# Optimization experiments

Hardware: AMD Instinct MI355X
Metric: run time of the kernel (lower is better)

## Reference

```python
import jax, jax.numpy as jnp
from jax import lax
import numpy as np

N_NODES = 50000
N_EDGES = 800000
IN_CH = 128
HEADS = 4
OUT_CH = 32
TOP_K = 8


def setup_inputs() -> dict:
    key = jax.random.key(0)
    k1, k2, k3, k4 = jax.random.split(key, 4)
    x = jax.random.normal(k1, (N_NODES, IN_CH), jnp.float32)
    edge_index = jax.random.randint(k2, (2, N_EDGES), 0, N_NODES, dtype=jnp.int32)
    scale = float(np.sqrt(2.0 / (IN_CH + HEADS * OUT_CH)))  # xavier-ish
    W = jax.random.normal(k3, (IN_CH, HEADS * OUT_CH), jnp.float32) * scale
    att = jax.random.normal(k4, (HEADS, 2 * OUT_CH), jnp.float32) * 0.1
    return {"x": x, "W": W, "att": att, "edge_index": edge_index}


def _topk_mask_1h(e_h, row, k):
    # e_h: [E'] scores for one head; keep top-k scores within each row-segment.
    E = e_h.shape[0]
    order = jnp.lexsort((-e_h, row))          # grouped by row, descending score
    srow = row[order]
    seg_start = jnp.searchsorted(srow, srow, side="left")
    pos_in_seg = jnp.arange(E, dtype=seg_start.dtype) - seg_start
    keep_sorted = pos_in_seg < k
    return jnp.zeros((E,), jnp.bool_).at[order].set(keep_sorted)


def reference(x, W, att, edge_index):
    N = x.shape[0]
    H, C = HEADS, OUT_CH
    h = (x @ W).reshape(N, H, C)              # [N,H,C]
    # add self loops
    loops = jnp.arange(N, dtype=edge_index.dtype)
    ei = jnp.concatenate([edge_index, jnp.stack([loops, loops])], axis=1)
    row, col = ei[0], ei[1]                   # [E']
    x_i = h[row]                              # [E',H,C] gather (dst)
    x_j = h[col]                              # [E',H,C] gather (src)
    a_i, a_j = att[:, :C], att[:, C:]
    e = jnp.einsum("ehc,hc->eh", x_i, a_i) + jnp.einsum("ehc,hc->eh", x_j, a_j)
    e = jax.nn.leaky_relu(e, negative_slope=0.2)  # [E',H]
    mask = jax.vmap(lambda eh: _topk_mask_1h(eh, row, TOP_K),
                    in_axes=1, out_axes=1)(e)     # [E',H] bool
    e = jnp.where(mask, e, -jnp.inf)
    # segment softmax over rows (every node has a self loop -> non-empty segment)
    seg_max = jax.ops.segment_max(e, row, num_segments=N)
    ez = jnp.exp(e - lax.stop_gradient(seg_max)[row])  # masked edges -> 0
    denom = jax.ops.segment_sum(ez, row, num_segments=N)
    alpha = ez / denom[row]                   # [E',H]
    # dropout is identity in eval mode
    out = jax.ops.segment_sum(alpha[:, :, None] * x_j, row, num_segments=N)
    out = out.reshape(N, H * C)               # concat=True
    return jax.nn.elu(out)
```

## Files before the change

### kernel.cpp

```cpp
#include <hip/hip_runtime.h>
#include <math.h>

typedef unsigned int u32;
typedef unsigned long long u64;

#define NN 50000
#define NE 800000
#define TOPK 8
#define NB 196
#define BCAP 4608
#define CURSTRIDE 16
#define GTILES 782
#define PBLOCKS 391

__global__ __launch_bounds__(256) void gemm_k(const float* __restrict__ x,
                                              const float* __restrict__ W,
                                              const float* __restrict__ att,
                                              float* __restrict__ hbuf,
                                              float* __restrict__ s_i,
                                              float* __restrict__ s_j,
                                              int* __restrict__ cursor) {
    __shared__ float xst[64][68];
    __shared__ float ws[64][128];
    const int t = threadIdx.x;
    const int cx = t & 15;
    const int ry = t >> 4;
    const int rbase = blockIdx.x * 64;

    if (blockIdx.x == 0 && t < NB) cursor[t * CURSTRIDE] = 0;

    float acc[4][8];
    #pragma unroll
    for (int i = 0; i < 4; ++i)
        #pragma unroll
        for (int j = 0; j < 8; ++j) acc[i][j] = 0.f;

    for (int kk = 0; kk < 128; kk += 64) {
        if (kk) __syncthreads();
        #pragma unroll
        for (int rr = ry; rr < 64; rr += 16) {
            int gr = rbase + rr;
            float4 v = make_float4(0.f, 0.f, 0.f, 0.f);
            if (gr < NN)
                v = *reinterpret_cast<const float4*>(x + (size_t)gr * 128 + kk + cx * 4);
            xst[cx * 4 + 0][rr] = v.x;
            xst[cx * 4 + 1][rr] = v.y;
            xst[cx * 4 + 2][rr] = v.z;
            xst[cx * 4 + 3][rr] = v.w;
        }
        #pragma unroll
        for (int wk = t >> 5; wk < 64; wk += 8) {
            float4 v = *reinterpret_cast<const float4*>(W + (size_t)(kk + wk) * 128 + (t & 31) * 4);
            *reinterpret_cast<float4*>(&ws[wk][(t & 31) * 4]) = v;
        }
        __syncthreads();

        for (int k = 0; k < 64; ++k) {
            float4 xa = *reinterpret_cast<const float4*>(&xst[k][ry * 4]);
            float4 wa = *reinterpret_cast<const float4*>(&ws[k][cx * 8]);
            float4 wb = *reinterpret_cast<const float4*>(&ws[k][cx * 8 + 4]);
            float xv[4] = {xa.x, xa.y, xa.z, xa.w};
            float wv[8] = {wa.x, wa.y, wa.z, wa.w, wb.x, wb.y, wb.z, wb.w};
            #pragma unroll
            for (int i = 0; i < 4; ++i)
                #pragma unroll
                for (int j = 0; j < 8; ++j) acc[i][j] += xv[i] * wv[j];
        }
    }

    const int head = cx >> 2;
    float aiv[8], ajv[8];
    #pragma unroll
    for (int j = 0; j < 8; ++j) {
        aiv[j] = att[head * 64 + (cx & 3) * 8 + j];
        ajv[j] = att[head * 64 + 32 + (cx & 3) * 8 + j];
    }
    #pragma unroll
    for (int i = 0; i < 4; ++i) {
        int gr = rbase + ry * 4 + i;
        float pi = 0.f, pj = 0.f;
        #pragma unroll
        for (int j = 0; j < 8; ++j) {
            pi += acc[i][j] * aiv[j];
            pj += acc[i][j] * ajv[j];
        }
        pi += __shfl_xor(pi, 1); pi += __shfl_xor(pi, 2);
        pj += __shfl_xor(pj, 1); pj += __shfl_xor(pj, 2);
        if (gr < NN) {
            float* dst = hbuf + (size_t)gr * 128 + cx * 8;
            *reinterpret_cast<float4*>(dst)     = make_float4(acc[i][0], acc[i][1], acc[i][2], acc[i][3]);
            *reinterpret_cast<float4*>(dst + 4) = make_float4(acc[i][4], acc[i][5], acc[i][6], acc[i][7]);
            if ((cx & 3) == 0) {
                s_i[(size_t)gr * 4 + head] = pi;
                s_j[(size_t)gr * 4 + head] = pj;
            }
        }
    }
}

__global__ __launch_bounds__(256) void part_k(const int* __restrict__ ei,
                                              int* __restrict__ cursor,
                                              u32* __restrict__ breg) {
    __shared__ u32 cnt[NB];
    __shared__ u32 base[NB];
    const int t = threadIdx.x;
    if (t < NB) cnt[t] = 0;
    __syncthreads();

    const int e0 = blockIdx.x * 2048 + t * 8;
    const bool ev = e0 < NE;
    int rows[8], cols[8], bk[8];
    u32 lrk[8];
    if (ev) {
        int4 ra = *reinterpret_cast<const int4*>(ei + e0);
        int4 rb = *reinterpret_cast<const int4*>(ei + e0 + 4);
        int4 ca = *reinterpret_cast<const int4*>(ei + NE + e0);
        int4 cb = *reinterpret_cast<const int4*>(ei + NE + e0 + 4);
        rows[0] = ra.x; rows[1] = ra.y; rows[2] = ra.z; rows[3] = ra.w;
        rows[4] = rb.x; rows[5] = rb.y; rows[6] = rb.z; rows[7] = rb.w;
        cols[0] = ca.x; cols[1] = ca.y; cols[2] = ca.z; cols[3] = ca.w;
        cols[4] = cb.x; cols[5] = cb.y; cols[6] = cb.z; cols[7] = cb.w;
        #pragma unroll
        for (int i = 0; i < 8; ++i) {
            bk[i] = rows[i] >> 8;
            lrk[i] = atomicAdd(&cnt[bk[i]], 1u);
        }
    }
    __syncthreads();
    if (t < NB) base[t] = (cnt[t] > 0) ? (u32)atomicAdd(cursor + t * CURSTRIDE, (int)cnt[t]) : 0u;
    __syncthreads();
    if (ev) {
        #pragma unroll
        for (int i = 0; i < 8; ++i) {
            u32 pos = base[bk[i]] + lrk[i];
            if (pos < BCAP)
                breg[(size_t)bk[i] * BCAP + pos] = ((u32)(rows[i] & 255) << 16) | (u32)cols[i];
        }
    }
}

__global__ __launch_bounds__(256) void rowsel_k(const int* __restrict__ cursor,
                                                const u32* __restrict__ breg,
                                                const float* __restrict__ s_i,
                                                const float* __restrict__ s_j,
                                                const float* __restrict__ hbuf,
                                                float* __restrict__ out) {
    __shared__ u32 lcsr[64][65];
    __shared__ u32 ldeg[64];
    __shared__ float lal[256 * 8];
    __shared__ int   lcl[256 * 8];
    const int t = threadIdx.x;
    const int B = blockIdx.x >> 2;
    const int s = blockIdx.x & 3;
    const int rbase = B * 256 + s * 64;

    if (t < 64) ldeg[t] = 0;
    __syncthreads();

    int n = cursor[B * CURSTRIDE];
    if (n > BCAP) n = BCAP;
    const u32* reg = breg + (size_t)B * BCAP;
    for (int i = t; i < n; i += 256) {
        u32 e = reg[i];
        if ((int)(e >> 22) == s) {
            int lr = (int)((e >> 16) & 63);
            u32 rk = atomicAdd(&ldeg[lr], 1u);
            if (rk < 64) lcsr[lr][rk] = e & 0xFFFFu;
        }
    }
    __syncthreads();

    const int lrow = t >> 2;
    const int head = t & 3;
    const int row = rbase + lrow;

    u64 kl[TOPK];
    int cl[TOPK];
    #pragma unroll
    for (int i = 0; i < TOPK; ++i) { kl[i] = 0ull; cl[i] = 0; }

    int dgr = 0;
    if (row < NN) {
        dgr = (int)ldeg[lrow];
        if (dgr > 64) dgr = 64;
        float v = s_j[(size_t)row * 4 + head];
        u32 b = __float_as_uint(v);
        u32 fk = (b & 0x80000000u) ? ~b : (b | 0x80000000u);
        kl[0] = ((u64)fk << 32) | (u32)(~(u32)(NE + row));
        cl[0] = row;
    }

    for (int j = 0; j < dgr; ++j) {
        int col = (int)lcsr[lrow][j];
        float v = s_j[(size_t)col * 4 + head];
        u32 b = __float_as_uint(v);
        u32 fk = (b & 0x80000000u) ? ~b : (b | 0x80000000u);
        u64 key = ((u64)fk << 32) | (u32)(~(u32)j);
        int cc = col;
        if (key > kl[TOPK - 1]) {
            #pragma unroll
            for (int i = 0; i < TOPK; ++i) {
                bool gt = key > kl[i];
                u64 tk = gt ? kl[i] : key;  kl[i] = gt ? key : kl[i];  key = tk;
                int tc = gt ? cl[i] : cc;   cl[i] = gt ? cc : cl[i];   cc = tc;
            }
        }
    }

    {
        float si = (row < NN) ? s_i[(size_t)row * 4 + head] : 0.f;
        u32 fk = (u32)(kl[0] >> 32);
        u32 b = (fk & 0x80000000u) ? (fk ^ 0x80000000u) : ~fk;
        float vmax = __uint_as_float(b);
        float em = si + vmax;
        float m = (em >= 0.f) ? em : 0.2f * em;
        float al[TOPK];
        float denom = 0.f;
        #pragma unroll
        for (int i = 0; i < TOPK; ++i) {
            u32 fki = (u32)(kl[i] >> 32);
            u32 bi = (fki & 0x80000000u) ? (fki ^ 0x80000000u) : ~fki;
            float v = __uint_as_float(bi);
            float e = si + v;
            e = (e >= 0.f) ? e : 0.2f * e;
            float z = (kl[i] != 0ull) ? __expf(e - m) : 0.f;
            al[i] = z;
            denom += z;
        }
        float inv = 1.f / denom;
        #pragma unroll
        for (int i = 0; i < TOPK; ++i) {
            lal[t * 8 + i] = al[i] * inv;
            lcl[t * 8 + i] = cl[i];
        }
    }
    __syncthreads();

    const int lane = t & 63;
    const int wid = t >> 6;
    const int q = lane >> 3;
    const int dq = lane & 7;
    for (int g = wid; g < 32; g += 4) {
        const int p = g * 8 + q;
        const int r = rbase + (p >> 2);
        const int hh = p & 3;
        if (r < NN) {
            const int base = p * 8;
            float av[8]; int cv[8];
            #pragma unroll
            for (int k = 0; k < 8; ++k) { av[k] = lal[base + k]; cv[k] = lcl[base + k]; }
            float4 a4 = make_float4(0.f, 0.f, 0.f, 0.f);
            #pragma unroll
            for (int k = 0; k < 8; ++k) {
                const float4 hv = *reinterpret_cast<const float4*>(
                    &hbuf[(size_t)cv[k] * 128 + hh * 32 + dq * 4]);
                a4.x += av[k] * hv.x;
                a4.y += av[k] * hv.y;
                a4.z += av[k] * hv.z;
                a4.w += av[k] * hv.w;
            }
            a4.x = (a4.x > 0.f) ? a4.x : expm1f(a4.x);
            a4.y = (a4.y > 0.f) ? a4.y : expm1f(a4.y);
            a4.z = (a4.z > 0.f) ? a4.z : expm1f(a4.z);
            a4.w = (a4.w > 0.f) ? a4.w : expm1f(a4.w);
            *reinterpret_cast<float4*>(&out[(size_t)r * 128 + hh * 32 + dq * 4]) = a4;
        }
    }
}

extern "C" void kernel_launch(void* const* d_in, const int* in_sizes, int n_in,
                              void* d_out, int out_size, void* d_ws, size_t ws_size,
                              hipStream_t stream) {
    const float* x   = (const float*)d_in[0];
    const float* W   = (const float*)d_in[1];
    const float* att = (const float*)d_in[2];
    const int*   ei  = (const int*)d_in[3];
    float* out = (float*)d_out;

    u32* breg    = (u32*)d_ws;
    float* hbuf  = (float*)(breg + (size_t)NB * BCAP);
    float* s_i   = hbuf + 6400000;
    float* s_j   = s_i + 200000;
    int* cursor  = (int*)(s_j + 200000);

    gemm_k<<<GTILES, 256, 0, stream>>>(x, W, att, hbuf, s_i, s_j, cursor);
    part_k<<<PBLOCKS, 256, 0, stream>>>(ei, cursor, breg);
    rowsel_k<<<NB * 4, 256, 0, stream>>>(cursor, breg, s_i, s_j, hbuf, out);
}
```

Before: 173.6 us.

## Fuse edge partitioning into GEMM kernel and shrink shared index arrays to u16

Edge bucketing moves out of the separate partition kernel and into the GEMM kernel. Each of the 782 GEMM blocks handles 1024 edges: it counts them in shared memory during the first K-step, reserves space with global cursor atomics during the second, and scatters after the epilogue. Cursor zeroing becomes a memset, which removes one kernel launch and overlaps the edge loads with GEMM compute. The rowsel kernel also stores column indices in 16-bit shared arrays to cut LDS footprint, at the cost of adding shared-memory pressure and a memset call to the GEMM path.

```diff
diff --git a/kernel.cpp b/kernel.cpp
--- a/kernel.cpp
+++ b/kernel.cpp
@@ -2,6 +2,7 @@
 #include <math.h>
 
 typedef unsigned int u32;
+typedef unsigned short u16;
 typedef unsigned long long u64;
 
 #define NN 50000
@@ -11,23 +12,37 @@
 #define BCAP 4608
 #define CURSTRIDE 16
 #define GTILES 782
-#define PBLOCKS 391
 
 __global__ __launch_bounds__(256) void gemm_k(const float* __restrict__ x,
                                               const float* __restrict__ W,
                                               const float* __restrict__ att,
+                                              const int* __restrict__ ei,
                                               float* __restrict__ hbuf,
                                               float* __restrict__ s_i,
                                               float* __restrict__ s_j,
-                                              int* __restrict__ cursor) {
+                                              int* __restrict__ cursor,
+                                              u32* __restrict__ breg) {
     __shared__ float xst[64][68];
     __shared__ float ws[64][128];
+    __shared__ u32 cnt[NB];
+    __shared__ u32 base[NB];
     const int t = threadIdx.x;
     const int cx = t & 15;
     const int ry = t >> 4;
     const int rbase = blockIdx.x * 64;
 
-    if (blockIdx.x == 0 && t < NB) cursor[t * CURSTRIDE] = 0;
+    const int e0 = blockIdx.x * 1024 + t * 4;
+    const bool ev = e0 < NE;
+    int4 er = make_int4(0, 0, 0, 0), ec = make_int4(0, 0, 0, 0);
+    if (ev) {
+        er = *reinterpret_cast<const int4*>(ei + e0);
+        ec = *reinterpret_cast<const int4*>(ei + NE + e0);
+    }
+    if (t < NB) cnt[t] = 0;
+
+    int bk[4];
+    u32 lrk[4] = {0, 0, 0, 0};
+    u32 myBase = 0;
 
     float acc[4][8];
     #pragma unroll
@@ -55,6 +70,20 @@
         }
         __syncthreads();
 
+        if (kk == 0) {
+            if (ev) {
+                int rows[4] = {er.x, er.y, er.z, er.w};
+                #pragma unroll
+                for (int i = 0; i < 4; ++i) {
+                    bk[i] = rows[i] >> 8;
+                    lrk[i] = atomicAdd(&cnt[bk[i]], 1u);
+                }
+            }
+        } else {
+            if (t < NB && cnt[t] > 0)
+                myBase = (u32)atomicAdd(cursor + t * CURSTRIDE, (int)cnt[t]);
+        }
+
         for (int k = 0; k < 64; ++k) {
             float4 xa = *reinterpret_cast<const float4*>(&xst[k][ry * 4]);
             float4 wa = *reinterpret_cast<const float4*>(&ws[k][cx * 8]);
@@ -96,42 +125,14 @@
             }
         }
     }
-}
-
-__global__ __launch_bounds__(256) void part_k(const int* __restrict__ ei,
-                                              int* __restrict__ cursor,
-                                              u32* __restrict__ breg) {
-    __shared__ u32 cnt[NB];
-    __shared__ u32 base[NB];
-    const int t = threadIdx.x;
-    if (t < NB) cnt[t] = 0;
-    __syncthreads();
-
-    const int e0 = blockIdx.x * 2048 + t * 8;
-    const bool ev = e0 < NE;
-    int rows[8], cols[8], bk[8];
-    u32 lrk[8];
+
+    if (t < NB) base[t] = myBase;
+    __syncthreads();
     if (ev) {
-        int4 ra = *reinterpret_cast<const int4*>(ei + e0);
-        int4 rb = *reinterpret_cast<const int4*>(ei + e0 + 4);
-        int4 ca = *reinterpret_cast<const int4*>(ei + NE + e0);
-        int4 cb = *reinterpret_cast<const int4*>(ei + NE + e0 + 4);
-        rows[0] = ra.x; rows[1] = ra.y; rows[2] = ra.z; rows[3] = ra.w;
-        rows[4] = rb.x; rows[5] = rb.y; rows[6] = rb.z; rows[7] = rb.w;
-        cols[0] = ca.x; cols[1] = ca.y; cols[2] = ca.z; cols[3] = ca.w;
-        cols[4] = cb.x; cols[5] = cb.y; cols[6] = cb.z; cols[7] = cb.w;
-        #pragma unroll
-        for (int i = 0; i < 8; ++i) {
-            bk[i] = rows[i] >> 8;
-            lrk[i] = atomicAdd(&cnt[bk[i]], 1u);
-        }
-    }
-    __syncthreads();
-    if (t < NB) base[t] = (cnt[t] > 0) ? (u32)atomicAdd(cursor + t * CURSTRIDE, (int)cnt[t]) : 0u;
-    __syncthreads();
-    if (ev) {
-        #pragma unroll
-        for (int i = 0; i < 8; ++i) {
+        int rows[4] = {er.x, er.y, er.z, er.w};
+        int cols[4] = {ec.x, ec.y, ec.z, ec.w};
+        #pragma unroll
+        for (int i = 0; i < 4; ++i) {
             u32 pos = base[bk[i]] + lrk[i];
             if (pos < BCAP)
                 breg[(size_t)bk[i] * BCAP + pos] = ((u32)(rows[i] & 255) << 16) | (u32)cols[i];
@@ -145,10 +146,10 @@
                                                 const float* __restrict__ s_j,
                                                 const float* __restrict__ hbuf,
                                                 float* __restrict__ out) {
-    __shared__ u32 lcsr[64][65];
+    __shared__ u16 lcsr[64][66];
     __shared__ u32 ldeg[64];
     __shared__ float lal[256 * 8];
-    __shared__ int   lcl[256 * 8];
+    __shared__ u16  lcl[256 * 8];
     const int t = threadIdx.x;
     const int B = blockIdx.x >> 2;
     const int s = blockIdx.x & 3;
@@ -165,7 +166,7 @@
         if ((int)(e >> 22) == s) {
             int lr = (int)((e >> 16) & 63);
             u32 rk = atomicAdd(&ldeg[lr], 1u);
-            if (rk < 64) lcsr[lr][rk] = e & 0xFFFFu;
+            if (rk < 64) lcsr[lr][rk] = (u16)(e & 0xFFFFu);
         }
     }
     __syncthreads();
@@ -231,7 +232,7 @@
         #pragma unroll
         for (int i = 0; i < TOPK; ++i) {
             lal[t * 8 + i] = al[i] * inv;
-            lcl[t * 8 + i] = cl[i];
+            lcl[t * 8 + i] = (u16)cl[i];
         }
     }
     __syncthreads();
@@ -248,7 +249,7 @@
             const int base = p * 8;
             float av[8]; int cv[8];
             #pragma unroll
-            for (int k = 0; k < 8; ++k) { av[k] = lal[base + k]; cv[k] = lcl[base + k]; }
+            for (int k = 0; k < 8; ++k) { av[k] = lal[base + k]; cv[k] = (int)lcl[base + k]; }
             float4 a4 = make_float4(0.f, 0.f, 0.f, 0.f);
             #pragma unroll
             for (int k = 0; k < 8; ++k) {
@@ -283,7 +284,7 @@
     float* s_j   = s_i + 200000;
     int* cursor  = (int*)(s_j + 200000);
 
-    gemm_k<<<GTILES, 256, 0, stream>>>(x, W, att, hbuf, s_i, s_j, cursor);
-    part_k<<<PBLOCKS, 256, 0, stream>>>(ei, cursor, breg);
+    hipMemsetAsync(cursor, 0, NB * CURSTRIDE * sizeof(int), stream);
+    gemm_k<<<GTILES, 256, 0, stream>>>(x, W, att, ei, hbuf, s_i, s_j, cursor, breg);
     rowsel_k<<<NB * 4, 256, 0, stream>>>(cursor, breg, s_i, s_j, hbuf, out);
 }
```

Result: faster. 167.8 us (-3.3%).
